# Kernel tuning notes

Measured on AMD Instinct MI355X. Metric: run time of the kernel, lower is better.

Reference implementation:

```python
import jax, jax.numpy as jnp
import numpy as np

NUM_Q = 4096  # C.NUM_OF_QUESTIONS
MAX_STEP = 200  # C.MAX_STEP
B = 64
EPS = 1e-8


def setup_inputs() -> dict:
    key = jax.random.key(0)
    k1, k2 = jax.random.split(key)
    # pred: probabilities in (0,1), shape [B, MAX_STEP-1, NUM_Q]
    pred = jax.random.uniform(k1, (B, MAX_STEP - 1, NUM_Q), dtype=jnp.float32)
    # batch: binary response encoding, shape [B, MAX_STEP, 2*NUM_Q]
    batch = jax.random.bernoulli(k2, 0.5, (B, MAX_STEP, 2 * NUM_Q)).astype(jnp.float32)
    return {"pred": pred, "batch": batch}


def reference(pred, batch):
    # Targets at t+1 aligned with predictions at t.
    tgt = batch[:, 1:MAX_STEP, :]            # [B, T-1, 2*NUM_Q]
    mask_q = tgt[..., :NUM_Q]                # answered correctly -> -log(p)
    mask_nq = tgt[..., NUM_Q:]               # answered incorrectly -> -log(1-p)
    loss = -jnp.sum(mask_q * jnp.log(pred + EPS) + mask_nq * jnp.log(1.0 - pred + EPS))
    return loss
```

## Files before the change

kernel.cpp:

```cpp
#include <hip/hip_runtime.h>

#define NUM_Q 4096
#define MAX_STEP 200
#define NBATCH 64
#define NT 199
#define EPS 1e-8f

__global__ __launch_bounds__(256) void loss_kernel(const float* __restrict__ pred,
                                                   const float* __restrict__ batch,
                                                   float* __restrict__ out) {
    const int row = blockIdx.x;
    const int b = row / NT;
    const int t = row % NT;

    const float4* __restrict__ predRow =
        (const float4*)(pred + (size_t)row * NUM_Q);
    const float* batchRow =
        batch + ((size_t)b * MAX_STEP + (size_t)(t + 1)) * (size_t)(2 * NUM_Q);
    const float4* __restrict__ mqRow  = (const float4*)(batchRow);
    const float4* __restrict__ mnqRow = (const float4*)(batchRow + NUM_Q);

    float acc = 0.0f;
    #pragma unroll
    for (int i = 0; i < 4; ++i) {
        const int idx = threadIdx.x + i * 256;
        float4 p  = predRow[idx];
        float4 mq = mqRow[idx];
        float4 mn = mnqRow[idx];
        acc += mq.x * __logf(p.x + EPS) + mn.x * __logf(1.0f - p.x + EPS);
        acc += mq.y * __logf(p.y + EPS) + mn.y * __logf(1.0f - p.y + EPS);
        acc += mq.z * __logf(p.z + EPS) + mn.z * __logf(1.0f - p.z + EPS);
        acc += mq.w * __logf(p.w + EPS) + mn.w * __logf(1.0f - p.w + EPS);
    }

    #pragma unroll
    for (int off = 32; off > 0; off >>= 1)
        acc += __shfl_down(acc, off, 64);

    __shared__ float smem[4];
    const int lane = threadIdx.x & 63;
    const int wave = threadIdx.x >> 6;
    if (lane == 0) smem[wave] = acc;
    __syncthreads();
    if (threadIdx.x == 0) {
        float s = smem[0] + smem[1] + smem[2] + smem[3];
        atomicAdd(out, -s);
    }
}

extern "C" void kernel_launch(void* const* d_in, const int* in_sizes, int n_in,
                              void* d_out, int out_size, void* d_ws, size_t ws_size,
                              hipStream_t stream) {
    const float* pred  = (const float*)d_in[0];
    const float* batch = (const float*)d_in[1];
    float* out = (float*)d_out;

    hipMemsetAsync(out, 0, sizeof(float), stream);

    loss_kernel<<<NBATCH * NT, 256, 0, stream>>>(pred, batch, out);
}
```

Measured before the change: 690.5 us.

## Use grid-stride persistent blocks with two-pass reduction instead of per-row atomics

Replaces one block per (batch,time) row with a fixed grid of 1024 blocks that grid-stride over all float4 elements, so each block writes a partial sum to workspace. A second single-block kernel then reduces the partial sums and writes the negated loss, which removes the memset and the roughly 12.7k same-address atomic adds. The cost is an extra kernel launch, and the loop has no unrolling, so fewer loads may be in flight per thread.

```diff
diff --git a/kernel.cpp b/kernel.cpp
--- a/kernel.cpp
+++ b/kernel.cpp
@@ -5,28 +5,28 @@
 #define NBATCH 64
 #define NT 199
 #define EPS 1e-8f
+#define NQ4 (NUM_Q / 4)
+#define TOTAL_V4 (NBATCH * NT * NQ4)
+#define NBLK 1024
 
-__global__ __launch_bounds__(256) void loss_kernel(const float* __restrict__ pred,
-                                                   const float* __restrict__ batch,
-                                                   float* __restrict__ out) {
-    const int row = blockIdx.x;
-    const int b = row / NT;
-    const int t = row % NT;
-
-    const float4* __restrict__ predRow =
-        (const float4*)(pred + (size_t)row * NUM_Q);
-    const float* batchRow =
-        batch + ((size_t)b * MAX_STEP + (size_t)(t + 1)) * (size_t)(2 * NUM_Q);
-    const float4* __restrict__ mqRow  = (const float4*)(batchRow);
-    const float4* __restrict__ mnqRow = (const float4*)(batchRow + NUM_Q);
+__global__ __launch_bounds__(256) void loss_main(const float* __restrict__ pred,
+                                                 const float* __restrict__ batch,
+                                                 float* __restrict__ blockSums) {
+    const float4* __restrict__ pred4 = (const float4*)pred;
+    const int stride = NBLK * 256;
 
     float acc = 0.0f;
-    #pragma unroll
-    for (int i = 0; i < 4; ++i) {
-        const int idx = threadIdx.x + i * 256;
-        float4 p  = predRow[idx];
-        float4 mq = mqRow[idx];
-        float4 mn = mnqRow[idx];
+    for (int g = blockIdx.x * 256 + threadIdx.x; g < TOTAL_V4; g += stride) {
+        const int row = g >> 10;
+        const int r   = g & (NQ4 - 1);
+        const int b   = row / NT;
+        const int t   = row - b * NT;
+        const float4* __restrict__ bq =
+            (const float4*)(batch + ((size_t)(b * MAX_STEP + t + 1) << 13));
+
+        float4 p  = pred4[g];
+        float4 mq = bq[r];
+        float4 mn = bq[r + NQ4];
         acc += mq.x * __logf(p.x + EPS) + mn.x * __logf(1.0f - p.x + EPS);
         acc += mq.y * __logf(p.y + EPS) + mn.y * __logf(1.0f - p.y + EPS);
         acc += mq.z * __logf(p.z + EPS) + mn.z * __logf(1.0f - p.z + EPS);
@@ -42,10 +42,28 @@
     const int wave = threadIdx.x >> 6;
     if (lane == 0) smem[wave] = acc;
     __syncthreads();
-    if (threadIdx.x == 0) {
-        float s = smem[0] + smem[1] + smem[2] + smem[3];
-        atomicAdd(out, -s);
-    }
+    if (threadIdx.x == 0)
+        blockSums[blockIdx.x] = smem[0] + smem[1] + smem[2] + smem[3];
+}
+
+__global__ __launch_bounds__(256) void loss_final(const float* __restrict__ blockSums,
+                                                  float* __restrict__ out) {
+    float acc = 0.0f;
+    #pragma unroll
+    for (int k = 0; k < NBLK / 256; ++k)
+        acc += blockSums[threadIdx.x + k * 256];
+
+    #pragma unroll
+    for (int off = 32; off > 0; off >>= 1)
+        acc += __shfl_down(acc, off, 64);
+
+    __shared__ float smem[4];
+    const int lane = threadIdx.x & 63;
+    const int wave = threadIdx.x >> 6;
+    if (lane == 0) smem[wave] = acc;
+    __syncthreads();
+    if (threadIdx.x == 0)
+        out[0] = -(smem[0] + smem[1] + smem[2] + smem[3]);
 }
 
 extern "C" void kernel_launch(void* const* d_in, const int* in_sizes, int n_in,
@@ -53,9 +71,9 @@
                               hipStream_t stream) {
     const float* pred  = (const float*)d_in[0];
     const float* batch = (const float*)d_in[1];
-    float* out = (float*)d_out;
+    float* blockSums   = (float*)d_ws;
+    float* out         = (float*)d_out;
 
-    hipMemsetAsync(out, 0, sizeof(float), stream);
-
-    loss_kernel<<<NBATCH * NT, 256, 0, stream>>>(pred, batch, out);
+    loss_main<<<NBLK, 256, 0, stream>>>(pred, batch, blockSums);
+    loss_final<<<1, 256, 0, stream>>>(blockSums, out);
 }
```

Result: faster. 640.9 us (-7.2%).
